# Kernel optimization log

Hardware: AMD Instinct MI355X
Metric: run time of the kernel (lower is better)

Reference implementation:

```python
import jax, jax.numpy as jnp
import numpy as np

N = 8192          # num_nodes (adj.shape[0])
NFEAT = 1433      # Cora features
NHID = 64
NCLASS = 7
P_VEC_SIZE = N * (N + 1) // 2  # lower triangle incl. diagonal


def setup_inputs() -> dict:
    key = jax.random.key(0)
    k1, k2, k3, k4 = jax.random.split(key, 4)
    x = jax.random.normal(k1, (N, NFEAT), dtype=jnp.float32)
    # sparse symmetric 0/1 adjacency, avg degree ~33
    u = jax.random.uniform(k2, (N, N), dtype=jnp.float32)
    a = (u < 0.002).astype(jnp.float32)
    sub_adj = jnp.clip(a + a.T, 0.0, 1.0)
    sub_adj = sub_adj * (1.0 - jnp.eye(N, dtype=jnp.float32))  # no self loops
    # P_vec initialized to ones (edge_additions=False branch), minus eps as in reset_parameters
    P_vec = jnp.ones((P_VEC_SIZE,), dtype=jnp.float32)
    W1 = jax.random.normal(k3, (NFEAT, NHID), dtype=jnp.float32) / np.sqrt(NFEAT)
    b1 = jnp.zeros((NHID,), dtype=jnp.float32)
    W2 = jax.random.normal(k4, (NHID, NCLASS), dtype=jnp.float32) / np.sqrt(NHID)
    b2 = jnp.zeros((NCLASS,), dtype=jnp.float32)
    return {"x": x, "sub_adj": sub_adj, "P_vec": P_vec,
            "W1": W1, "b1": b1, "W2": W2, "b2": b2}


def _symm_from_vec(p_vec, n):
    # create_symm_matrix_from_vec: scatter vec into lower triangle (incl diag),
    # then mirror strict lower triangle to upper.
    il, jl = jnp.tril_indices(n)
    m = jnp.zeros((n, n), dtype=p_vec.dtype).at[il, jl].set(p_vec)
    return jnp.tril(m) + jnp.tril(m, -1).T


def reference(x, sub_adj, P_vec, W1, b1, W2, b2):
    n = sub_adj.shape[0]
    P_hat_symm = _symm_from_vec(P_vec, n)
    # A_tilde = sigmoid(P) * sub_adj + I  (edge_additions=False)
    A_tilde = jax.nn.sigmoid(P_hat_symm) * sub_adj + jnp.eye(n, dtype=sub_adj.dtype)
    # degree matrix is detached in the original forward
    d = jax.lax.stop_gradient(jnp.sum(A_tilde, axis=1))
    d_inv_sqrt = jnp.where(d > 0, d ** -0.5, 0.0)  # inf -> 0 guard
    # D^-1/2 A D^-1/2 (diag matmuls expressed as broadcasts)
    norm_adj = d_inv_sqrt[:, None] * A_tilde * d_inv_sqrt[None, :]
    # 2-layer GCN (pygcn GraphConvolution: adj @ (x @ W) + b); eval mode => dropout is identity
    h1 = jax.nn.relu(norm_adj @ (x @ W1) + b1)
    h2 = norm_adj @ (h1 @ W2) + b2
    return jax.nn.log_softmax(h2, axis=1)
```

## Files before the change

### kernel.cpp

```cpp
#include <hip/hip_runtime.h>
#include <hip/hip_bf16.h>
#include <math.h>

#define NN 8192
#define NFEAT 1433
#define NHID 64
#define NCLASS 7
#define CAP 96

#define KSPLIT 8
#define KCHUNK 180
#define NB_GEMM 1024
#define NB_BUILD 2048
#define KT 32
#define XSS 66

typedef float f32x4 __attribute__((ext_vector_type(4)));

__global__ __launch_bounds__(256, 8) void k_fused(const float* __restrict__ adj,
                                                  const float* __restrict__ P,
                                                  const float* __restrict__ x,
                                                  const float* __restrict__ W1,
                                                  float* __restrict__ dinv,
                                                  int* __restrict__ cnt,
                                                  int* __restrict__ cols,
                                                  float* __restrict__ vals,
                                                  float* __restrict__ part) {
    __shared__ float xs[KT][XSS];
    __shared__ float ws[KT][64];

    const int t = threadIdx.x;
    const int b = blockIdx.x;
    const int rmod = b % 3;
    const int g = b / 3;

    if (rmod == 0) {
        const int tile = g >> 3;
        const int ks   = g & 7;
        const int m0 = tile * 64;
        const int k_begin = ks * KCHUNK;
        const int k_end   = (k_begin + KCHUNK < NFEAT) ? k_begin + KCHUNK : NFEAT;
        const int r0 = (t & 15) * 4;
        const int c0 = (t >> 4) * 4;
        float acc[4][4] = {};

        for (int k0 = k_begin; k0 < k_end; k0 += KT) {
            #pragma unroll
            for (int i = 0; i < 8; ++i) {
                int e = t + 256 * i;
                int r = e >> 5, kk = e & 31;
                int k = k0 + kk;
                xs[kk][r] = (k < k_end)
                    ? __builtin_nontemporal_load(x + (size_t)(m0 + r) * NFEAT + k)
                    : 0.f;
            }
            {
                int kk = t >> 4, c4 = (t & 15) * 4;
                #pragma unroll
                for (int i = 0; i < 2; ++i) {
                    int kkk = kk + 16 * i;
                    int k = k0 + kkk;
                    float4 w = (k < k_end) ? *(const float4*)(W1 + (size_t)k * 64 + c4)
                                           : make_float4(0.f, 0.f, 0.f, 0.f);
                    *(float4*)(&ws[kkk][c4]) = w;
                }
            }
            __syncthreads();
            #pragma unroll
            for (int kk = 0; kk < KT; ++kk) {
                float2 a01 = *(const float2*)(&xs[kk][r0]);
                float2 a23 = *(const float2*)(&xs[kk][r0 + 2]);
                float4 bv  = *(const float4*)(&ws[kk][c0]);
                float a[4] = {a01.x, a01.y, a23.x, a23.y};
                float bb[4] = {bv.x, bv.y, bv.z, bv.w};
                #pragma unroll
                for (int i = 0; i < 4; ++i)
                    #pragma unroll
                    for (int j = 0; j < 4; ++j)
                        acc[i][j] += a[i] * bb[j];
            }
            __syncthreads();
        }
        float* pout = part + (size_t)ks * NN * NHID;
        #pragma unroll
        for (int i = 0; i < 4; ++i) {
            float4 o = make_float4(acc[i][0], acc[i][1], acc[i][2], acc[i][3]);
            *(float4*)(&pout[(size_t)(m0 + r0 + i) * 64 + c0]) = o;
        }
    } else {
        const int wave = t >> 6;
        const int lane = t & 63;
        const int bid  = 2 * g + (rmod - 1);
        const int row  = bid * 4 + wave;

        const f32x4* arow4 = (const f32x4*)(adj + (size_t)row * NN);
        const long tb = (long)row * (row + 1) / 2;
        const unsigned long long lt = (1ull << lane) - 1ull;
        const size_t rowCAP = (size_t)row * CAP;

        int base = 0;
        float dsum = 0.f;

        f32x4 buf[4];
        #pragma unroll
        for (int i = 0; i < 4; ++i)
            buf[i] = __builtin_nontemporal_load(&arow4[i * 64 + lane]);

        for (int sb = 0; sb < 8; ++sb) {
            f32x4 cur[4];
            #pragma unroll
            for (int i = 0; i < 4; ++i) cur[i] = buf[i];
            if (sb < 7) {
                #pragma unroll
                for (int i = 0; i < 4; ++i)
                    buf[i] = __builtin_nontemporal_load(&arow4[((sb + 1) * 4 + i) * 64 + lane]);
            }
            #pragma unroll
            for (int i = 0; i < 4; ++i) {
                const int jb = ((sb * 4 + i) * 64 + lane) * 4;
                #pragma unroll
                for (int s = 0; s < 4; ++s) {
                    float av = cur[i][s];
                    bool nz = (av != 0.f);
                    unsigned long long mask = __ballot(nz);
                    if (nz) {
                        int j = jb + s;
                        long pidx = (j <= row) ? (tb + j) : ((long)j * (j + 1) / 2 + row);
                        float p = P[pidx];
                        float v = av / (1.f + __expf(-p));
                        int pos = base + __popcll(mask & lt);
                        if (pos < CAP) {
                            cols[rowCAP + pos] = j;
                            vals[rowCAP + pos] = v;
                        }
                        dsum += v;
                    }
                    base += __popcll(mask);
                }
            }
        }
        #pragma unroll
        for (int s = 32; s; s >>= 1) dsum += __shfl_xor(dsum, s, 64);
        if (lane == 0) {
            cnt[row]  = (base < CAP) ? base : CAP;
            dinv[row] = 1.f / sqrtf(1.f + dsum);
        }
    }
}

__global__ __launch_bounds__(256) void k_reduce(const float* __restrict__ part,
                                                float* __restrict__ XW1) {
    const size_t i4 = (size_t)blockIdx.x * 256 + threadIdx.x;
    const f32x4* p4 = (const f32x4*)part;
    f32x4 s = p4[i4];
    #pragma unroll
    for (int ks = 1; ks < KSPLIT; ++ks)
        s += p4[(size_t)ks * (NN * NHID / 4) + i4];
    ((f32x4*)XW1)[i4] = s;
}

__global__ __launch_bounds__(256) void k_spmm1(const float* __restrict__ XW1,
                                               const float* __restrict__ dinv,
                                               const int* __restrict__ cnt,
                                               const int* __restrict__ cols,
                                               const float* __restrict__ vals,
                                               const float* __restrict__ b1,
                                               const float* __restrict__ W2,
                                               float* __restrict__ HW2) {
    const int wave = threadIdx.x >> 6;
    const int lane = threadIdx.x & 63;
    const int row  = blockIdx.x * 4 + wave;
    if (row >= NN) return;

    const float di = dinv[row];
    float acc = di * XW1[(size_t)row * NHID + lane];
    const int c = cnt[row];
    const int*   cp = cols + (size_t)row * CAP;
    const float* vp = vals + (size_t)row * CAP;

    int jn = 0; float vn = 0.f;
    if (c > 0) { jn = cp[0]; vn = vp[0]; }
    for (int k = 0; k < c; ++k) {
        int j = jn; float v = vn;
        if (k + 1 < c) { jn = cp[k + 1]; vn = vp[k + 1]; }
        acc += v * dinv[j] * XW1[(size_t)j * NHID + lane];
    }
    float h1 = di * acc + b1[lane];
    h1 = fmaxf(h1, 0.f);

    float o[NCLASS];
    #pragma unroll
    for (int cc = 0; cc < NCLASS; ++cc) o[cc] = h1 * W2[lane * NCLASS + cc];
    #pragma unroll
    for (int cc = 0; cc < NCLASS; ++cc)
        for (int s = 32; s; s >>= 1) o[cc] += __shfl_xor(o[cc], s, 64);
    if (lane == 0) {
        #pragma unroll
        for (int cc = 0; cc < NCLASS; ++cc)
            HW2[(size_t)row * NCLASS + cc] = o[cc];
    }
}

__global__ __launch_bounds__(256) void k_spmm2(const float* __restrict__ HW2,
                                               const float* __restrict__ dinv,
                                               const int* __restrict__ cnt,
                                               const int* __restrict__ cols,
                                               const float* __restrict__ vals,
                                               const float* __restrict__ b2,
                                               float* __restrict__ out) {
    const int wave = threadIdx.x >> 6;
    const int lane = threadIdx.x & 63;
    const int row  = blockIdx.x * 4 + wave;
    if (row >= NN) return;

    const int c = cnt[row];
    const int*   cp = cols + (size_t)row * CAP;
    const float* vp = vals + (size_t)row * CAP;
    float acc[NCLASS] = {};
    for (int k = lane; k < c; k += 64) {
        int j   = cp[k];
        float w = vp[k] * dinv[j];
        #pragma unroll
        for (int cc = 0; cc < NCLASS; ++cc)
            acc[cc] += w * HW2[(size_t)j * NCLASS + cc];
    }
    #pragma unroll
    for (int cc = 0; cc < NCLASS; ++cc)
        for (int s = 32; s; s >>= 1) acc[cc] += __shfl_xor(acc[cc], s, 64);

    if (lane == 0) {
        const float di = dinv[row];
        float h[NCLASS], m = -1e30f;
        #pragma unroll
        for (int cc = 0; cc < NCLASS; ++cc) {
            h[cc] = di * (acc[cc] + di * HW2[(size_t)row * NCLASS + cc]) + b2[cc];
            m = fmaxf(m, h[cc]);
        }
        float s = 0.f;
        #pragma unroll
        for (int cc = 0; cc < NCLASS; ++cc) s += expf(h[cc] - m);
        float lse = m + logf(s);
        #pragma unroll
        for (int cc = 0; cc < NCLASS; ++cc)
            out[(size_t)row * NCLASS + cc] = h[cc] - lse;
    }
}

extern "C" void kernel_launch(void* const* d_in, const int* in_sizes, int n_in,
                              void* d_out, int out_size, void* d_ws, size_t ws_size,
                              hipStream_t stream) {
    const float* x   = (const float*)d_in[0];
    const float* adj = (const float*)d_in[1];
    const float* P   = (const float*)d_in[2];
    const float* W1  = (const float*)d_in[3];
    const float* b1  = (const float*)d_in[4];
    const float* W2  = (const float*)d_in[5];
    const float* b2  = (const float*)d_in[6];
    float* out = (float*)d_out;

    char* ws = (char*)d_ws;
    const size_t SZ_DINV = (size_t)NN * 4;
    const size_t SZ_CNT  = (size_t)NN * 4;
    const size_t SZ_COLS = (size_t)NN * CAP * 4;
    const size_t SZ_VALS = (size_t)NN * CAP * 4;
    const size_t SZ_XW1  = (size_t)NN * NHID * 4;

    float* dinv = (float*)ws;
    int*   cnt  = (int*)  (ws + SZ_DINV);
    int*   cols = (int*)  (ws + SZ_DINV + SZ_CNT);
    float* vals = (float*)(ws + SZ_DINV + SZ_CNT + SZ_COLS);
    float* XW1  = (float*)(ws + SZ_DINV + SZ_CNT + SZ_COLS + SZ_VALS);
    float* HW2  = (float*)(ws + SZ_DINV + SZ_CNT + SZ_COLS + SZ_VALS + SZ_XW1);
    float* part = (float*)(ws + SZ_DINV + SZ_CNT + SZ_COLS + SZ_VALS + SZ_XW1 +
                           (size_t)NN * NCLASS * 4 + 256);

    k_fused<<<dim3(NB_GEMM + NB_BUILD), dim3(256), 0, stream>>>(adj, P, x, W1,
                                                                dinv, cnt, cols, vals, part);
    k_reduce<<<dim3(NN * NHID / 4 / 256), dim3(256), 0, stream>>>(part, XW1);
    k_spmm1<<<dim3(NN / 4), dim3(256), 0, stream>>>(XW1, dinv, cnt, cols, vals, b1, W2, HW2);
    k_spmm2<<<dim3(NN / 4), dim3(256), 0, stream>>>(HW2, dinv, cnt, cols, vals, b2, out);
}
```

Baseline: 134.2 us.

## Use bf16 MFMA for X@W1, defer sigmoid gather, deepen spmm1 prefetch

The dense X@W1 split-K GEMM moves from fp32 FMA register tiling to bf16 MFMA 16x16x32, with x converted to bf16 on the fly and W1 pre-transposed to bf16 by a new prep kernel. The adjacency build pass now records only column indices during the ballot scan and then gathers P and computes sigmoids in a compact second loop, instead of doing divergent P loads inside the scan. spmm1 prefetches two neighbours ahead, including the XW1 and dinv values. The bf16 inputs reduce precision of the first layer, and the extra launch adds overhead.

```diff
diff --git a/kernel.cpp b/kernel.cpp
--- a/kernel.cpp
+++ b/kernel.cpp
@@ -9,25 +9,40 @@
 #define CAP 96
 
 #define KSPLIT 8
-#define KCHUNK 180
+#define KCHUNK 192
+#define KPAD 1440
 #define NB_GEMM 1024
 #define NB_BUILD 2048
-#define KT 32
-#define XSS 66
 
 typedef float f32x4 __attribute__((ext_vector_type(4)));
+typedef short bf16x8 __attribute__((ext_vector_type(8)));
+
+__device__ __forceinline__ ushort f2bf(float f) {
+    __hip_bfloat16 h = __float2bfloat16(f);
+    return *reinterpret_cast<ushort*>(&h);
+}
+
+__global__ __launch_bounds__(256) void k_prep(const float* __restrict__ W1,
+                                              ushort* __restrict__ W1bfT) {
+    int idx = blockIdx.x * 256 + threadIdx.x;
+    if (idx >= KPAD * 64) return;
+    int k = idx >> 6, c = idx & 63;
+    W1bfT[(size_t)c * KPAD + k] = (k < NFEAT) ? f2bf(W1[(size_t)k * 64 + c]) : (ushort)0;
+}
 
 __global__ __launch_bounds__(256, 8) void k_fused(const float* __restrict__ adj,
                                                   const float* __restrict__ P,
                                                   const float* __restrict__ x,
-                                                  const float* __restrict__ W1,
+                                                  const ushort* __restrict__ W1bfT,
                                                   float* __restrict__ dinv,
                                                   int* __restrict__ cnt,
                                                   int* __restrict__ cols,
                                                   float* __restrict__ vals,
                                                   float* __restrict__ part) {
-    __shared__ float xs[KT][XSS];
-    __shared__ float ws[KT][64];
+    __shared__ __align__(16) union SMem {
+        struct { ushort xa[64][40]; ushort wt[64][40]; } g;
+        int bcols[4][CAP];
+    } sm;
 
     const int t = threadIdx.x;
     const int b = blockIdx.x;
@@ -40,53 +55,57 @@
         const int m0 = tile * 64;
         const int k_begin = ks * KCHUNK;
         const int k_end   = (k_begin + KCHUNK < NFEAT) ? k_begin + KCHUNK : NFEAT;
-        const int r0 = (t & 15) * 4;
-        const int c0 = (t >> 4) * 4;
-        float acc[4][4] = {};
-
-        for (int k0 = k_begin; k0 < k_end; k0 += KT) {
+        const int l = t & 63;
+        const int w = t >> 6;
+
+        const int sr  = t >> 2;
+        const int sc8 = (t & 3) * 8;
+        const float* xrow = x + (size_t)(m0 + sr) * NFEAT;
+        const int wc  = t & 63;
+        const int wk8 = (t >> 6) * 8;
+        const ushort* wsrc = W1bfT + (size_t)wc * KPAD;
+        const int arow = w * 16 + (l & 15);
+        const int kb   = (l >> 4) * 8;
+
+        f32x4 acc[4];
+        #pragma unroll
+        for (int ct = 0; ct < 4; ++ct) acc[ct] = (f32x4){0.f, 0.f, 0.f, 0.f};
+
+        for (int k0 = k_begin; k0 < k_end; k0 += 32) {
+            uint4 xp;
+            {
+                ushort u[8];
+                #pragma unroll
+                for (int jj = 0; jj < 8; ++jj) {
+                    int k = k0 + sc8 + jj;
+                    float f = (k < k_end) ? xrow[k] : 0.f;
+                    u[jj] = f2bf(f);
+                }
+                xp.x = (unsigned)u[0] | ((unsigned)u[1] << 16);
+                xp.y = (unsigned)u[2] | ((unsigned)u[3] << 16);
+                xp.z = (unsigned)u[4] | ((unsigned)u[5] << 16);
+                xp.w = (unsigned)u[6] | ((unsigned)u[7] << 16);
+            }
+            *(uint4*)(&sm.g.xa[sr][sc8]) = xp;
+            *(uint4*)(&sm.g.wt[wc][wk8]) = *(const uint4*)(wsrc + k0 + wk8);
+            __syncthreads();
+
+            bf16x8 af = *(const bf16x8*)(&sm.g.xa[arow][kb]);
             #pragma unroll
-            for (int i = 0; i < 8; ++i) {
-                int e = t + 256 * i;
-                int r = e >> 5, kk = e & 31;
-                int k = k0 + kk;
-                xs[kk][r] = (k < k_end)
-                    ? __builtin_nontemporal_load(x + (size_t)(m0 + r) * NFEAT + k)
-                    : 0.f;
-            }
-            {
-                int kk = t >> 4, c4 = (t & 15) * 4;
-                #pragma unroll
-                for (int i = 0; i < 2; ++i) {
-                    int kkk = kk + 16 * i;
-                    int k = k0 + kkk;
-                    float4 w = (k < k_end) ? *(const float4*)(W1 + (size_t)k * 64 + c4)
-                                           : make_float4(0.f, 0.f, 0.f, 0.f);
-                    *(float4*)(&ws[kkk][c4]) = w;
-                }
+            for (int ct = 0; ct < 4; ++ct) {
+                bf16x8 bfr = *(const bf16x8*)(&sm.g.wt[ct * 16 + (l & 15)][kb]);
+                acc[ct] = __builtin_amdgcn_mfma_f32_16x16x32_bf16(af, bfr, acc[ct], 0, 0, 0);
             }
             __syncthreads();
+        }
+        float* pout = part + (size_t)ks * NN * NHID;
+        const int orow = m0 + w * 16 + ((l >> 4) << 2);
+        const int ocol = l & 15;
+        #pragma unroll
+        for (int ct = 0; ct < 4; ++ct)
             #pragma unroll
-            for (int kk = 0; kk < KT; ++kk) {
-                float2 a01 = *(const float2*)(&xs[kk][r0]);
-                float2 a23 = *(const float2*)(&xs[kk][r0 + 2]);
-                float4 bv  = *(const float4*)(&ws[kk][c0]);
-                float a[4] = {a01.x, a01.y, a23.x, a23.y};
-                float bb[4] = {bv.x, bv.y, bv.z, bv.w};
-                #pragma unroll
-                for (int i = 0; i < 4; ++i)
-                    #pragma unroll
-                    for (int j = 0; j < 4; ++j)
-                        acc[i][j] += a[i] * bb[j];
-            }
-            __syncthreads();
-        }
-        float* pout = part + (size_t)ks * NN * NHID;
-        #pragma unroll
-        for (int i = 0; i < 4; ++i) {
-            float4 o = make_float4(acc[i][0], acc[i][1], acc[i][2], acc[i][3]);
-            *(float4*)(&pout[(size_t)(m0 + r0 + i) * 64 + c0]) = o;
-        }
+            for (int rix = 0; rix < 4; ++rix)
+                pout[(size_t)(orow + rix) * 64 + ct * 16 + ocol] = acc[ct][rix];
     } else {
         const int wave = t >> 6;
         const int lane = t & 63;
@@ -99,7 +118,6 @@
         const size_t rowCAP = (size_t)row * CAP;
 
         int base = 0;
-        float dsum = 0.f;
 
         f32x4 buf[4];
         #pragma unroll
@@ -120,29 +138,36 @@
                 const int jb = ((sb * 4 + i) * 64 + lane) * 4;
                 #pragma unroll
                 for (int s = 0; s < 4; ++s) {
-                    float av = cur[i][s];
-                    bool nz = (av != 0.f);
+                    bool nz = (cur[i][s] != 0.f);
                     unsigned long long mask = __ballot(nz);
                     if (nz) {
                         int j = jb + s;
-                        long pidx = (j <= row) ? (tb + j) : ((long)j * (j + 1) / 2 + row);
-                        float p = P[pidx];
-                        float v = av / (1.f + __expf(-p));
                         int pos = base + __popcll(mask & lt);
                         if (pos < CAP) {
                             cols[rowCAP + pos] = j;
-                            vals[rowCAP + pos] = v;
+                            sm.bcols[wave][pos] = j;
                         }
-                        dsum += v;
                     }
                     base += __popcll(mask);
                 }
             }
         }
+        __syncthreads();
+
+        const int c = (base < CAP) ? base : CAP;
+        float dsum = 0.f;
+        for (int k = lane; k < c; k += 64) {
+            int j = sm.bcols[wave][k];
+            long pidx = (j <= row) ? (tb + j) : ((long)j * (j + 1) / 2 + row);
+            float p = P[pidx];
+            float v = 1.f / (1.f + __expf(-p));
+            vals[rowCAP + k] = v;
+            dsum += v;
+        }
         #pragma unroll
         for (int s = 32; s; s >>= 1) dsum += __shfl_xor(dsum, s, 64);
         if (lane == 0) {
-            cnt[row]  = (base < CAP) ? base : CAP;
+            cnt[row]  = c;
             dinv[row] = 1.f / sqrtf(1.f + dsum);
         }
     }
@@ -178,12 +203,18 @@
     const int*   cp = cols + (size_t)row * CAP;
     const float* vp = vals + (size_t)row * CAP;
 
-    int jn = 0; float vn = 0.f;
-    if (c > 0) { jn = cp[0]; vn = vp[0]; }
+    int j0 = 0, j1 = 0; float v0 = 0.f, v1 = 0.f, w0 = 0.f, w1 = 0.f, d0 = 0.f, d1 = 0.f;
+    if (c > 0) { j0 = cp[0]; v0 = vp[0]; w0 = XW1[(size_t)j0 * NHID + lane]; d0 = dinv[j0]; }
+    if (c > 1) { j1 = cp[1]; v1 = vp[1]; w1 = XW1[(size_t)j1 * NHID + lane]; d1 = dinv[j1]; }
     for (int k = 0; k < c; ++k) {
-        int j = jn; float v = vn;
-        if (k + 1 < c) { jn = cp[k + 1]; vn = vp[k + 1]; }
-        acc += v * dinv[j] * XW1[(size_t)j * NHID + lane];
+        acc += v0 * d0 * w0;
+        j0 = j1; v0 = v1; w0 = w1; d0 = d1;
+        if (k + 2 < c) {
+            int jn = cp[k + 2];
+            j1 = jn; v1 = vp[k + 2];
+            w1 = XW1[(size_t)jn * NHID + lane];
+            d1 = dinv[jn];
+        }
     }
     float h1 = di * acc + b1[lane];
     h1 = fmaxf(h1, 0.f);
@@ -219,10 +250,10 @@
     float acc[NCLASS] = {};
     for (int k = lane; k < c; k += 64) {
         int j   = cp[k];
-        float w = vp[k] * dinv[j];
+        float wgt = vp[k] * dinv[j];
         #pragma unroll
         for (int cc = 0; cc < NCLASS; ++cc)
-            acc[cc] += w * HW2[(size_t)j * NCLASS + cc];
+            acc[cc] += wgt * HW2[(size_t)j * NCLASS + cc];
     }
     #pragma unroll
     for (int cc = 0; cc < NCLASS; ++cc)
@@ -259,22 +290,18 @@
     float* out = (float*)d_out;
 
     char* ws = (char*)d_ws;
-    const size_t SZ_DINV = (size_t)NN * 4;
-    const size_t SZ_CNT  = (size_t)NN * 4;
-    const size_t SZ_COLS = (size_t)NN * CAP * 4;
-    const size_t SZ_VALS = (size_t)NN * CAP * 4;
-    const size_t SZ_XW1  = (size_t)NN * NHID * 4;
-
-    float* dinv = (float*)ws;
-    int*   cnt  = (int*)  (ws + SZ_DINV);
-    int*   cols = (int*)  (ws + SZ_DINV + SZ_CNT);
-    float* vals = (float*)(ws + SZ_DINV + SZ_CNT + SZ_COLS);
-    float* XW1  = (float*)(ws + SZ_DINV + SZ_CNT + SZ_COLS + SZ_VALS);
-    float* HW2  = (float*)(ws + SZ_DINV + SZ_CNT + SZ_COLS + SZ_VALS + SZ_XW1);
-    float* part = (float*)(ws + SZ_DINV + SZ_CNT + SZ_COLS + SZ_VALS + SZ_XW1 +
-                           (size_t)NN * NCLASS * 4 + 256);
-
-    k_fused<<<dim3(NB_GEMM + NB_BUILD), dim3(256), 0, stream>>>(adj, P, x, W1,
+    size_t off = 0;
+    float* dinv = (float*)(ws + off);  off += (size_t)NN * 4;
+    int*   cnt  = (int*)  (ws + off);  off += (size_t)NN * 4;
+    int*   cols = (int*)  (ws + off);  off += (size_t)NN * CAP * 4;
+    float* vals = (float*)(ws + off);  off += (size_t)NN * CAP * 4;
+    float* XW1  = (float*)(ws + off);  off += (size_t)NN * NHID * 4;
+    float* HW2  = (float*)(ws + off);  off += (size_t)NN * NCLASS * 4;
+    float* part = (float*)(ws + off);  off += (size_t)KSPLIT * NN * NHID * 4;
+    ushort* W1bfT = (ushort*)(ws + off); off += (size_t)64 * KPAD * 2;
+
+    k_prep<<<dim3(KPAD * 64 / 256), dim3(256), 0, stream>>>(W1, W1bfT);
+    k_fused<<<dim3(NB_GEMM + NB_BUILD), dim3(256), 0, stream>>>(adj, P, x, W1bfT,
                                                                 dinv, cnt, cols, vals, part);
     k_reduce<<<dim3(NN * NHID / 4 / 256), dim3(256), 0, stream>>>(part, XW1);
     k_spmm1<<<dim3(NN / 4), dim3(256), 0, stream>>>(XW1, dinv, cnt, cols, vals, b1, W2, HW2);
```

Result: faster. 128.5 us (-4.2%).
